# Kernel tuning notes

Hardware: AMD Instinct MI355X
Metric: run time of the kernel (lower is better)

Reference implementation:

```python
import jax, jax.numpy as jnp
import numpy as np

WT_LEVELS = 3  # wavelet decomposition levels

def haar2d(x):
    # orthonormal 2D Haar: 2x2 block -> 4 sub-bands, each scaled by 1/2
    a = x[:, :, 0::2, 0::2]; b = x[:, :, 0::2, 1::2]
    c = x[:, :, 1::2, 0::2]; d = x[:, :, 1::2, 1::2]
    ll = (a + b + c + d) * 0.5
    lh = (a - b + c - d) * 0.5
    hl = (a + b - c - d) * 0.5
    hh = (a - b - c + d) * 0.5
    return jnp.stack([ll, lh, hl, hh], axis=2)  # [B,C,4,h,w]

def ihaar2d(co):
    # exact inverse of haar2d
    ll, lh, hl, hh = co[:, :, 0], co[:, :, 1], co[:, :, 2], co[:, :, 3]
    a = (ll + lh + hl + hh) * 0.5
    b = (ll - lh + hl - hh) * 0.5
    c = (ll + lh - hl - hh) * 0.5
    d = (ll - lh - hl + hh) * 0.5
    B, C, h, w = ll.shape
    top = jnp.stack([a, b], axis=-1).reshape(B, C, h, 2 * w)
    bot = jnp.stack([c, d], axis=-1).reshape(B, C, h, 2 * w)
    return jnp.stack([top, bot], axis=3).reshape(B, C, 2 * h, 2 * w)

def dwconv(x, w):
    # depthwise conv, stride 1, 'same' padding (matches torch padding='same', k=5)
    return jax.lax.conv_general_dilated(
        x, w, (1, 1), 'SAME',
        dimension_numbers=('NCHW', 'OIHW', 'NCHW'),
        feature_group_count=x.shape[1])

def setup_inputs() -> dict:
    key = jax.random.key(0)
    ks = jax.random.split(key, 5)
    B, C, H, W, K, L = 8, 96, 224, 224, 5, WT_LEVELS
    x = jax.random.normal(ks[0], (B, C, H, W), jnp.float32)
    base_w = jax.random.normal(ks[1], (C, 1, K, K), jnp.float32) * 0.1
    base_b = jax.random.normal(ks[2], (C,), jnp.float32) * 0.01
    base_scale = jnp.ones((1, C, 1, 1), jnp.float32)
    wconv_w = jax.random.normal(ks[3], (L, 4 * C, 1, K, K), jnp.float32) * 0.1
    wscale = jnp.full((L, 1, 4 * C, 1, 1), 0.1, jnp.float32)
    return {"x": x, "base_w": base_w, "base_b": base_b,
            "base_scale": base_scale, "wconv_w": wconv_w, "wscale": wscale}

def reference(x, base_w, base_b, base_scale, wconv_w, wscale):
    B, C, H, W = x.shape
    # analysis cascade: decompose LL of previous level, conv+scale all 4 bands
    cur = x
    level_coeffs = []
    for i in range(WT_LEVELS):
        co = haar2d(cur)                 # [B,C,4,h,w]
        cur = co[:, :, 0]                # pre-conv LL feeds next level
        h, w = co.shape[-2:]
        flat = co.reshape(B, C * 4, h, w)
        flat = dwconv(flat, wconv_w[i]) * wscale[i]
        level_coeffs.append(flat.reshape(B, C, 4, h, w))
    # synthesis cascade: reconstructed LL from deeper level is added to
    # the shallower level's (convolved) LL band before inverse transform
    next_ll = jnp.zeros_like(level_coeffs[-1][:, :, 0])
    for i in reversed(range(WT_LEVELS)):
        co = level_coeffs[i].at[:, :, 0].add(next_ll)
        next_ll = ihaar2d(co)
    base = dwconv(x, base_w) * base_scale + base_b.reshape(1, C, 1, 1)
    return base + next_ll
```

## Files before the change

### kernel.cpp

```cpp
#include <hip/hip_runtime.h>

#define BB 8
#define CC 96
#define HH 224
#define WW 224

typedef _Float16 h2 __attribute__((ext_vector_type(2)));
__device__ __forceinline__ h2 u2h(unsigned u) { return __builtin_bit_cast(h2, u); }
__device__ __forceinline__ unsigned pkrtz(float a, float b) {
    return __builtin_bit_cast(unsigned, __builtin_amdgcn_cvt_pkrtz(a, b));
}

#if __has_builtin(__builtin_amdgcn_fdot2)
#define FDOT2(a, b, c) __builtin_amdgcn_fdot2((a), (b), (c), false)
#else
#define FDOT2(a, b, c) ((float)(a).x * (float)(b).x + (float)(a).y * (float)(b).y + (c))
#endif

__global__ __launch_bounds__(512, 4) void levels_fused(
    const float* __restrict__ x,
    float* __restrict__ c1,
    float* __restrict__ c2,
    const float* __restrict__ wt1, const float* __restrict__ ws1,
    const float* __restrict__ wt2, const float* __restrict__ ws2)
{
    const int bc = blockIdx.x, c = bc % CC;
    const int t = threadIdx.x;

    __shared__ unsigned s_c1[112 * 58];
    __shared__ unsigned s_sb1[4 * 60 * 31];
    __shared__ unsigned s_cur2[56 * 30];
    __shared__ unsigned s_sb2[4 * 32 * 17];
    __shared__ unsigned s_w2[240];

    for (int i = t; i < 4 * 60 * 31; i += 512) s_sb1[i] = 0;
    for (int i = t; i < 4 * 32 * 17; i += 512) s_sb2[i] = 0;

    if (t < 80) {
        int knl = t / 10;
        int par = t & 1, row = (t % 10) >> 1;
        int lvl = knl >> 2, s = knl & 3;
        const float* wt  = lvl ? wt2 : wt1;
        const float* wsc = lvl ? ws2 : ws1;
        float sc = 0.5f * wsc[c * 4 + s];
        float wv[5];
        #pragma unroll
        for (int j = 0; j < 5; ++j) wv[j] = wt[(c * 4 + s) * 25 + row * 5 + j] * sc;
        unsigned* dst = &s_w2[(knl * 2 + par) * 15 + row * 3];
        if (par == 0) {
            dst[0] = pkrtz(wv[0], wv[1]);
            dst[1] = pkrtz(wv[2], wv[3]);
            dst[2] = pkrtz(wv[4], 0.f);
        } else {
            dst[0] = pkrtz(0.f, wv[0]);
            dst[1] = pkrtz(wv[1], wv[2]);
            dst[2] = pkrtz(wv[3], wv[4]);
        }
    }

    const float* xp = x + (size_t)bc * HH * WW;
    for (int idx = t; idx < 112 * 56; idx += 512) {
        int r = idx / 56, g = idx % 56;
        const float* r0 = xp + (size_t)(2 * r) * WW + 4 * g;
        const float* r1 = r0 + WW;
        float4 a = *(const float4*)r0;
        float4 b = *(const float4*)r1;
        s_c1[r * 58 + g] = pkrtz(0.5f * (a.x + a.y + b.x + b.y),
                                 0.5f * (a.z + a.w + b.z + b.w));
    }
    __syncthreads();

    for (int idx = t; idx < 56 * 28; idx += 512) {
        int sr = idx / 28, sc2 = idx % 28;
        uint2 tp = *(const uint2*)&s_c1[(2 * sr) * 58 + 2 * sc2];
        uint2 bt = *(const uint2*)&s_c1[(2 * sr + 1) * 58 + 2 * sc2];
        h2 t0 = u2h(tp.x), t1 = u2h(tp.y), b0 = u2h(bt.x), b1 = u2h(bt.y);
        float P0 = (float)t0.x + (float)t0.y, M0 = (float)t0.x - (float)t0.y;
        float R0 = (float)b0.x + (float)b0.y, Q0 = (float)b0.x - (float)b0.y;
        float P1 = (float)t1.x + (float)t1.y, M1 = (float)t1.x - (float)t1.y;
        float R1 = (float)b1.x + (float)b1.y, Q1 = (float)b1.x - (float)b1.y;
        int o = (sr + 2) * 31 + (sc2 + 1);
        s_sb1[0 * 1860 + o] = pkrtz(P0 + R0, P1 + R1);
        s_sb1[1 * 1860 + o] = pkrtz(M0 + Q0, M1 + Q1);
        s_sb1[2 * 1860 + o] = pkrtz(P0 - R0, P1 - R1);
        s_sb1[3 * 1860 + o] = pkrtz(M0 - Q0, M1 - Q1);
        s_cur2[sr * 30 + sc2] = pkrtz(0.5f * (P0 + R0), 0.5f * (P1 + R1));
    }
    __syncthreads();

    if (t < 28 * 14) {
        int sr = t / 14, sc2 = t % 14;
        uint2 tp = *(const uint2*)&s_cur2[(2 * sr) * 30 + 2 * sc2];
        uint2 bt = *(const uint2*)&s_cur2[(2 * sr + 1) * 30 + 2 * sc2];
        h2 t0 = u2h(tp.x), t1 = u2h(tp.y), b0 = u2h(bt.x), b1 = u2h(bt.y);
        float P0 = (float)t0.x + (float)t0.y, M0 = (float)t0.x - (float)t0.y;
        float R0 = (float)b0.x + (float)b0.y, Q0 = (float)b0.x - (float)b0.y;
        float P1 = (float)t1.x + (float)t1.y, M1 = (float)t1.x - (float)t1.y;
        float R1 = (float)b1.x + (float)b1.y, Q1 = (float)b1.x - (float)b1.y;
        int o = (sr + 2) * 17 + (sc2 + 1);
        s_sb2[0 * 544 + o] = pkrtz(P0 + R0, P1 + R1);
        s_sb2[1 * 544 + o] = pkrtz(M0 + Q0, M1 + Q1);
        s_sb2[2 * 544 + o] = pkrtz(P0 - R0, P1 - R1);
        s_sb2[3 * 544 + o] = pkrtz(M0 - Q0, M1 - Q1);
    }

    {
        const int s = t >> 7, lane = t & 127;
        const int q = lane & 63, half = lane >> 6;
        if (q < 56) {
            const int par = q & 1, d0 = q >> 1, ps = half * 28;
            h2 w[5][3];
            {
                const unsigned* wp = &s_w2[(s * 2 + par) * 15];
                #pragma unroll
                for (int ki = 0; ki < 5; ++ki)
                    #pragma unroll
                    for (int m = 0; m < 3; ++m) w[ki][m] = u2h(wp[ki * 3 + m]);
            }
            float acc[28];
            #pragma unroll
            for (int r = 0; r < 28; ++r) acc[r] = 0.f;
            #pragma unroll
            for (int ri = 0; ri < 32; ++ri) {
                const unsigned* rp = &s_sb1[s * 1860 + (ps + ri) * 31 + d0];
                h2 g0 = u2h(rp[0]), g1 = u2h(rp[1]), g2 = u2h(rp[2]);
                #pragma unroll
                for (int ki = 0; ki < 5; ++ki) {
                    int r = ri - ki;
                    if (r >= 0 && r < 28)
                        acc[r] = FDOT2(g0, w[ki][0],
                                 FDOT2(g1, w[ki][1],
                                 FDOT2(g2, w[ki][2], acc[r])));
                }
            }
            const size_t ob = ((size_t)(bc * 4 + s) * 56 + ps) * 56 + q;
            #pragma unroll
            for (int r = 0; r < 28; ++r)
                c1[ob + (size_t)r * 56] = acc[r];
        }
    }
    __syncthreads();

    if (t < 112) {
        const int s = t / 28, q = t % 28;
        const int par = q & 1, d0 = q >> 1;
        h2 w[5][3];
        {
            const unsigned* wp = &s_w2[((4 + s) * 2 + par) * 15];
            #pragma unroll
            for (int ki = 0; ki < 5; ++ki)
                #pragma unroll
                for (int m = 0; m < 3; ++m) w[ki][m] = u2h(wp[ki * 3 + m]);
        }
        float acc[28];
        #pragma unroll
        for (int r = 0; r < 28; ++r) acc[r] = 0.f;
        #pragma unroll
        for (int ri = 0; ri < 32; ++ri) {
            const unsigned* rp = &s_sb2[s * 544 + ri * 17 + d0];
            h2 g0 = u2h(rp[0]), g1 = u2h(rp[1]), g2 = u2h(rp[2]);
            #pragma unroll
            for (int ki = 0; ki < 5; ++ki) {
                int r = ri - ki;
                if (r >= 0 && r < 28)
                    acc[r] = FDOT2(g0, w[ki][0],
                             FDOT2(g1, w[ki][1],
                             FDOT2(g2, w[ki][2], acc[r])));
            }
        }
        const size_t ob = (size_t)(bc * 4 + s) * 28 * 28 + q;
        #pragma unroll
        for (int r = 0; r < 28; ++r)
            c2[ob + (size_t)r * 28] = acc[r];
    }
}

__global__ __launch_bounds__(256, 7) void final_fused_v5(
    const float* __restrict__ x,
    const float* __restrict__ bw,
    const float* __restrict__ bb,
    const float* __restrict__ bs,
    const float* __restrict__ wt0,
    const float* __restrict__ wsc0,
    const float* __restrict__ c1,
    const float* __restrict__ c2,
    float* __restrict__ out)
{
    const int bc = blockIdx.z, c = bc % CC;
    const int t = threadIdx.x;

    __shared__ unsigned s_x2[64 * 34];
    __shared__ unsigned s_sb[4 * 544];
    __shared__ float s_rec1[28 * 29];
    __shared__ float s_rec2[14 * 15];
    __shared__ unsigned s_w2[150];
    _Float16* const s_cvh = reinterpret_cast<_Float16*>(s_x2);

    if (t < 50) {
        int par = t & 1, row = (t >> 1) % 5, knl = t / 10;
        float wv[5];
        if (knl == 0) {
            float sc = bs[c];
            #pragma unroll
            for (int j = 0; j < 5; ++j) wv[j] = bw[c * 25 + row * 5 + j] * sc;
        } else {
            int s = knl - 1;
            float sc = 0.5f * wsc0[c * 4 + s];
            #pragma unroll
            for (int j = 0; j < 5; ++j) wv[j] = wt0[(c * 4 + s) * 25 + row * 5 + j] * sc;
        }
        unsigned* dst = &s_w2[((knl * 2 + par) * 5 + row) * 3];
        if (par == 0) {
            dst[0] = pkrtz(wv[0], wv[1]);
            dst[1] = pkrtz(wv[2], wv[3]);
            dst[2] = pkrtz(wv[4], 0.f);
        } else {
            dst[0] = pkrtz(0.f, wv[0]);
            dst[1] = pkrtz(wv[1], wv[2]);
            dst[2] = pkrtz(wv[3], wv[4]);
        }
    }

    float c2v[4], c1v[4];
    const int p1 = t / 14, q1 = t % 14;
    if (t < 49) {
        const int p2 = t / 7, q2 = t % 7;
        const size_t b2 = (((size_t)bc * 4) * 28 + 7 * blockIdx.y + p2) * 28
                        + 7 * blockIdx.x + q2;
        #pragma unroll
        for (int s = 0; s < 4; ++s) c2v[s] = c2[b2 + (size_t)s * 28 * 28];
    }
    if (t < 196) {
        const size_t b1 = (((size_t)bc * 4) * 56 + 14 * blockIdx.y + p1) * 56
                        + 14 * blockIdx.x + q1;
        #pragma unroll
        for (int s = 0; s < 4; ++s) c1v[s] = c1[b1 + (size_t)s * 56 * 56];
    }

    const float* xp = x + (size_t)bc * HH * WW;
    const int gy0 = 56 * blockIdx.y - 4, gx0 = 56 * blockIdx.x - 4;
    for (int idx = t; idx < 1024; idx += 256) {
        int r = idx >> 4, j = idx & 15;
        int gr = gy0 + r, gc = gx0 + 4 * j;
        float4 v = make_float4(0.f, 0.f, 0.f, 0.f);
        if (gr >= 0 && gr < HH && gc >= 0 && gc + 3 < WW)
            v = *(const float4*)(xp + (size_t)gr * WW + gc);
        uint2 pp;
        pp.x = pkrtz(v.x, v.y);
        pp.y = pkrtz(v.z, v.w);
        *(uint2*)&s_x2[r * 34 + 2 * j] = pp;
    }

    if (t < 49) {
        const int p2 = t / 7, q2 = t % 7;
        float ll = c2v[0], lh = c2v[1], hl = c2v[2], hh = c2v[3];
        float a  = 0.5f * (ll + lh + hl + hh);
        float b  = 0.5f * (ll - lh + hl - hh);
        float cv = 0.5f * (ll + lh - hl - hh);
        float d  = 0.5f * (ll - lh - hl + hh);
        float* rp = &s_rec2[(2 * p2) * 15 + 2 * q2];
        rp[0] = a; rp[1] = b; rp[15] = cv; rp[16] = d;
    }
    __syncthreads();

    for (int idx = t; idx < 512; idx += 256) {
        int sr = idx >> 4, g = idx & 15;
        uint2 tp = *(const uint2*)&s_x2[(2 * sr) * 34 + 2 * g];
        uint2 bt = *(const uint2*)&s_x2[(2 * sr + 1) * 34 + 2 * g];
        h2 t0 = u2h(tp.x), t1 = u2h(tp.y), b0 = u2h(bt.x), b1 = u2h(bt.y);
        float a0 = t0.x, e0 = t0.y, cc0 = b0.x, f0 = b0.y;
        float a1 = t1.x, e1 = t1.y, cc1 = b1.x, f1 = b1.y;
        float P0 = a0 + e0, M0 = a0 - e0, R0 = cc0 + f0, Q0 = cc0 - f0;
        float P1 = a1 + e1, M1 = a1 - e1, R1 = cc1 + f1, Q1 = cc1 - f1;
        s_sb[0 * 544 + sr * 17 + g] = pkrtz(P0 + R0, P1 + R1);
        s_sb[1 * 544 + sr * 17 + g] = pkrtz(M0 + Q0, M1 + Q1);
        s_sb[2 * 544 + sr * 17 + g] = pkrtz(P0 - R0, P1 - R1);
        s_sb[3 * 544 + sr * 17 + g] = pkrtz(M0 - Q0, M1 - Q1);
    }

    const int q4 = t % 56, rb4 = t / 56;
    float bacc[14];
    if (t < 224) {
        const int par = q4 & 1, d0 = (q4 + 2) >> 1;
        h2 w[5][3];
        {
            const unsigned* wp = &s_w2[(par * 5) * 3];
            #pragma unroll
            for (int ki = 0; ki < 5; ++ki)
                #pragma unroll
                for (int m = 0; m < 3; ++m) w[ki][m] = u2h(wp[ki * 3 + m]);
        }
        #pragma unroll
        for (int r = 0; r < 14; ++r) bacc[r] = 0.f;
        #pragma unroll
        for (int ri = 0; ri < 18; ++ri) {
            const unsigned* rp = &s_x2[(rb4 * 14 + ri + 2) * 34 + d0];
            h2 g0 = u2h(rp[0]), g1 = u2h(rp[1]), g2 = u2h(rp[2]);
            #pragma unroll
            for (int ki = 0; ki < 5; ++ki) {
                int r = ri - ki;
                if (r >= 0 && r < 14)
                    bacc[r] = FDOT2(g0, w[ki][0],
                              FDOT2(g1, w[ki][1],
                              FDOT2(g2, w[ki][2], bacc[r])));
            }
        }
    }
    if (t < 196) {
        float ll = c1v[0] + s_rec2[p1 * 15 + q1];
        float lh = c1v[1], hl = c1v[2], hh = c1v[3];
        float a  = 0.5f * (ll + lh + hl + hh);
        float b  = 0.5f * (ll - lh + hl - hh);
        float cv = 0.5f * (ll + lh - hl - hh);
        float d  = 0.5f * (ll - lh - hl + hh);
        float* rp = &s_rec1[(2 * p1) * 29 + 2 * q1];
        rp[0] = a; rp[1] = b; rp[29] = cv; rp[30] = d;
    }
    __syncthreads();

    {
        const int s = t >> 6, u = t & 63;
        if (u < 56) {
            const int q = u % 28, rb = u / 28;
            const int par = q & 1, d0 = q >> 1;
            h2 w[5][3];
            {
                const unsigned* wp = &s_w2[(((1 + s) * 2 + par) * 5) * 3];
                #pragma unroll
                for (int ki = 0; ki < 5; ++ki)
                    #pragma unroll
                    for (int m = 0; m < 3; ++m) w[ki][m] = u2h(wp[ki * 3 + m]);
            }
            float acc[14];
            #pragma unroll
            for (int r = 0; r < 14; ++r) acc[r] = 0.f;
            #pragma unroll
            for (int ri = 0; ri < 18; ++ri) {
                const unsigned* rp = &s_sb[s * 544 + (rb * 14 + ri) * 17 + d0];
                h2 g0 = u2h(rp[0]), g1 = u2h(rp[1]), g2 = u2h(rp[2]);
                #pragma unroll
                for (int ki = 0; ki < 5; ++ki) {
                    int r = ri - ki;
                    if (r >= 0 && r < 14)
                        acc[r] = FDOT2(g0, w[ki][0],
                                 FDOT2(g1, w[ki][1],
                                 FDOT2(g2, w[ki][2], acc[r])));
                }
            }
            #pragma unroll
            for (int r = 0; r < 14; ++r)
                s_cvh[(s * 28 + rb * 14 + r) * 29 + q] = (_Float16)acc[r];
        }
    }
    __syncthreads();

    if (t < 224) {
        const float bbv = bb[c];
        const int qs = q4 >> 1;
        const float sx = (q4 & 1) ? -1.f : 1.f;
        float* op = out + ((size_t)bc * HH + 56 * blockIdx.y + rb4 * 14) * WW
                        + 56 * blockIdx.x + q4;
        #pragma unroll
        for (int j = 0; j < 7; ++j) {
            const int p = rb4 * 7 + j;
            float ll = (float)s_cvh[(0 * 28 + p) * 29 + qs] + s_rec1[p * 29 + qs];
            float lh = (float)s_cvh[(1 * 28 + p) * 29 + qs];
            float hl = (float)s_cvh[(2 * 28 + p) * 29 + qs];
            float hh = (float)s_cvh[(3 * 28 + p) * 29 + qs];
            float e0 = ll + sx * lh;
            float e1 = hl + sx * hh;
            float top = 0.5f * (e0 + e1);
            float bot = 0.5f * (e0 - e1);
            op[(size_t)(2 * j) * WW]     = bacc[2 * j]     + bbv + top;
            op[(size_t)(2 * j + 1) * WW] = bacc[2 * j + 1] + bbv + bot;
        }
    }
}

extern "C" void kernel_launch(void* const* d_in, const int* in_sizes, int n_in,
                              void* d_out, int out_size, void* d_ws, size_t ws_size,
                              hipStream_t stream) {
    const float* x          = (const float*)d_in[0];
    const float* base_w     = (const float*)d_in[1];
    const float* base_b     = (const float*)d_in[2];
    const float* base_scale = (const float*)d_in[3];
    const float* wconv_w    = (const float*)d_in[4];
    const float* wscale     = (const float*)d_in[5];
    float* out = (float*)d_out;
    float* ws  = (float*)d_ws;

    const size_t n1 = (size_t)BB * CC * 4 * 56 * 56;

    float* coeffs1 = ws;
    float* coeffs2 = coeffs1 + n1;

    const int z = BB * CC;

    levels_fused<<<z, 512, 0, stream>>>(
        x, coeffs1, coeffs2,
        wconv_w + 1 * 384 * 25, wscale + 1 * 384,
        wconv_w + 2 * 384 * 25, wscale + 2 * 384);
    final_fused_v5<<<dim3(4, 4, z), 256, 0, stream>>>(
        x, base_w, base_b, base_scale,
        wconv_w + 0 * 384 * 25, wscale + 0 * 384, coeffs1, coeffs2, out);
}
```

Baseline: 147.8 us.

## Shrink final kernel tiles to 32x32 with single-wave 64-thread blocks

Retiles the final fused kernel from 56x56 output tiles with 256-thread blocks to 32x32 tiles with 64-thread blocks over a 7x7 grid per channel image. Every thread now does work, with no idle threads for t>=224 or the u>=56 gaps, and a block fits in one wavefront, so barriers are cheap and more blocks can be resident. In exchange, the 4-pixel halo is a larger share of each smaller tile, so global and LDS traffic per output pixel rises, and many more blocks must be scheduled.

```diff
diff --git a/kernel.cpp b/kernel.cpp
--- a/kernel.cpp
+++ b/kernel.cpp
@@ -175,7 +175,7 @@
     }
 }
 
-__global__ __launch_bounds__(256, 7) void final_fused_v5(
+__global__ __launch_bounds__(64) void final_fused_v6(
     const float* __restrict__ x,
     const float* __restrict__ bw,
     const float* __restrict__ bb,
@@ -188,13 +188,14 @@
 {
     const int bc = blockIdx.z, c = bc % CC;
     const int t = threadIdx.x;
-
-    __shared__ unsigned s_x2[64 * 34];
-    __shared__ unsigned s_sb[4 * 544];
-    __shared__ float s_rec1[28 * 29];
-    __shared__ float s_rec2[14 * 15];
+    const int ox = 32 * blockIdx.x, oy = 32 * blockIdx.y;
+
+    __shared__ unsigned s_x[40 * 22];
+    __shared__ unsigned s_sb[4 * 20 * 11];
+    __shared__ float s_rec1[16 * 17];
+    __shared__ float s_rec2[8 * 9];
     __shared__ unsigned s_w2[150];
-    _Float16* const s_cvh = reinterpret_cast<_Float16*>(s_x2);
+    _Float16* const s_cvh = reinterpret_cast<_Float16*>(s_x);
 
     if (t < 50) {
         int par = t & 1, row = (t >> 1) % 5, knl = t / 10;
@@ -222,66 +223,75 @@
     }
 
     float c2v[4], c1v[4];
-    const int p1 = t / 14, q1 = t % 14;
-    if (t < 49) {
-        const int p2 = t / 7, q2 = t % 7;
-        const size_t b2 = (((size_t)bc * 4) * 28 + 7 * blockIdx.y + p2) * 28
-                        + 7 * blockIdx.x + q2;
-        #pragma unroll
-        for (int s = 0; s < 4; ++s) c2v[s] = c2[b2 + (size_t)s * 28 * 28];
-    }
-    if (t < 196) {
-        const size_t b1 = (((size_t)bc * 4) * 56 + 14 * blockIdx.y + p1) * 56
-                        + 14 * blockIdx.x + q1;
-        #pragma unroll
-        for (int s = 0; s < 4; ++s) c1v[s] = c1[b1 + (size_t)s * 56 * 56];
+    if (t < 16) {
+        const int p2 = t >> 2, q2 = t & 3;
+        const size_t b2 = (((size_t)bc * 4) * 28 + 4 * blockIdx.y + p2) * 28
+                        + 4 * blockIdx.x + q2;
+        #pragma unroll
+        for (int s = 0; s < 4; ++s) c2v[s] = c2[b2 + (size_t)s * 784];
+    }
+    const int p1 = t >> 3, q1 = t & 7;
+    {
+        const size_t b1 = (((size_t)bc * 4) * 56 + 8 * blockIdx.y + p1) * 56
+                        + 8 * blockIdx.x + q1;
+        #pragma unroll
+        for (int s = 0; s < 4; ++s) c1v[s] = c1[b1 + (size_t)s * 3136];
     }
 
     const float* xp = x + (size_t)bc * HH * WW;
-    const int gy0 = 56 * blockIdx.y - 4, gx0 = 56 * blockIdx.x - 4;
-    for (int idx = t; idx < 1024; idx += 256) {
-        int r = idx >> 4, j = idx & 15;
-        int gr = gy0 + r, gc = gx0 + 4 * j;
-        float4 v = make_float4(0.f, 0.f, 0.f, 0.f);
-        if (gr >= 0 && gr < HH && gc >= 0 && gc + 3 < WW)
-            v = *(const float4*)(xp + (size_t)gr * WW + gc);
-        uint2 pp;
-        pp.x = pkrtz(v.x, v.y);
-        pp.y = pkrtz(v.z, v.w);
-        *(uint2*)&s_x2[r * 34 + 2 * j] = pp;
-    }
-
-    if (t < 49) {
-        const int p2 = t / 7, q2 = t % 7;
+    const int gy0 = oy - 4, gx0 = ox - 4;
+    #pragma unroll
+    for (int it = 0; it < 7; ++it) {
+        int idx = t + it * 64;
+        if (idx < 400) {
+            int r = idx / 10, j = idx % 10;
+            int gr = gy0 + r, gc = gx0 + 4 * j;
+            float4 v = make_float4(0.f, 0.f, 0.f, 0.f);
+            if (gr >= 0 && gr < HH && gc >= 0 && gc + 3 < WW)
+                v = *(const float4*)(xp + (size_t)gr * WW + gc);
+            uint2 pp;
+            pp.x = pkrtz(v.x, v.y);
+            pp.y = pkrtz(v.z, v.w);
+            *(uint2*)&s_x[r * 22 + 2 * j] = pp;
+        }
+    }
+
+    if (t < 16) {
+        const int p2 = t >> 2, q2 = t & 3;
         float ll = c2v[0], lh = c2v[1], hl = c2v[2], hh = c2v[3];
         float a  = 0.5f * (ll + lh + hl + hh);
         float b  = 0.5f * (ll - lh + hl - hh);
         float cv = 0.5f * (ll + lh - hl - hh);
         float d  = 0.5f * (ll - lh - hl + hh);
-        float* rp = &s_rec2[(2 * p2) * 15 + 2 * q2];
-        rp[0] = a; rp[1] = b; rp[15] = cv; rp[16] = d;
-    }
-    __syncthreads();
-
-    for (int idx = t; idx < 512; idx += 256) {
-        int sr = idx >> 4, g = idx & 15;
-        uint2 tp = *(const uint2*)&s_x2[(2 * sr) * 34 + 2 * g];
-        uint2 bt = *(const uint2*)&s_x2[(2 * sr + 1) * 34 + 2 * g];
-        h2 t0 = u2h(tp.x), t1 = u2h(tp.y), b0 = u2h(bt.x), b1 = u2h(bt.y);
-        float a0 = t0.x, e0 = t0.y, cc0 = b0.x, f0 = b0.y;
-        float a1 = t1.x, e1 = t1.y, cc1 = b1.x, f1 = b1.y;
-        float P0 = a0 + e0, M0 = a0 - e0, R0 = cc0 + f0, Q0 = cc0 - f0;
-        float P1 = a1 + e1, M1 = a1 - e1, R1 = cc1 + f1, Q1 = cc1 - f1;
-        s_sb[0 * 544 + sr * 17 + g] = pkrtz(P0 + R0, P1 + R1);
-        s_sb[1 * 544 + sr * 17 + g] = pkrtz(M0 + Q0, M1 + Q1);
-        s_sb[2 * 544 + sr * 17 + g] = pkrtz(P0 - R0, P1 - R1);
-        s_sb[3 * 544 + sr * 17 + g] = pkrtz(M0 - Q0, M1 - Q1);
-    }
-
-    const int q4 = t % 56, rb4 = t / 56;
-    float bacc[14];
-    if (t < 224) {
-        const int par = q4 & 1, d0 = (q4 + 2) >> 1;
+        float* rp = &s_rec2[(2 * p2) * 9 + 2 * q2];
+        rp[0] = a; rp[1] = b; rp[9] = cv; rp[10] = d;
+    }
+    __syncthreads();
+
+    #pragma unroll
+    for (int it = 0; it < 4; ++it) {
+        int idx = t + it * 64;
+        if (idx < 200) {
+            int sr = idx / 10, g = idx % 10;
+            uint2 tp = *(const uint2*)&s_x[(2 * sr) * 22 + 2 * g];
+            uint2 bt = *(const uint2*)&s_x[(2 * sr + 1) * 22 + 2 * g];
+            h2 t0 = u2h(tp.x), t1 = u2h(tp.y), b0 = u2h(bt.x), b1 = u2h(bt.y);
+            float P0 = (float)t0.x + (float)t0.y, M0 = (float)t0.x - (float)t0.y;
+            float R0 = (float)b0.x + (float)b0.y, Q0 = (float)b0.x - (float)b0.y;
+            float P1 = (float)t1.x + (float)t1.y, M1 = (float)t1.x - (float)t1.y;
+            float R1 = (float)b1.x + (float)b1.y, Q1 = (float)b1.x - (float)b1.y;
+            int o = sr * 11 + g;
+            s_sb[0 * 220 + o] = pkrtz(P0 + R0, P1 + R1);
+            s_sb[1 * 220 + o] = pkrtz(M0 + Q0, M1 + Q1);
+            s_sb[2 * 220 + o] = pkrtz(P0 - R0, P1 - R1);
+            s_sb[3 * 220 + o] = pkrtz(M0 - Q0, M1 - Q1);
+        }
+    }
+
+    const int qb = t & 31, hb = t >> 5;
+    float bacc[16];
+    {
+        const int par = qb & 1, d0 = (qb + 2) >> 1;
         h2 w[5][3];
         {
             const unsigned* wp = &s_w2[(par * 5) * 3];
@@ -291,82 +301,79 @@
                 for (int m = 0; m < 3; ++m) w[ki][m] = u2h(wp[ki * 3 + m]);
         }
         #pragma unroll
-        for (int r = 0; r < 14; ++r) bacc[r] = 0.f;
-        #pragma unroll
-        for (int ri = 0; ri < 18; ++ri) {
-            const unsigned* rp = &s_x2[(rb4 * 14 + ri + 2) * 34 + d0];
+        for (int r = 0; r < 16; ++r) bacc[r] = 0.f;
+        #pragma unroll
+        for (int ri = 0; ri < 20; ++ri) {
+            const unsigned* rp = &s_x[(hb * 16 + ri + 2) * 22 + d0];
             h2 g0 = u2h(rp[0]), g1 = u2h(rp[1]), g2 = u2h(rp[2]);
             #pragma unroll
             for (int ki = 0; ki < 5; ++ki) {
                 int r = ri - ki;
-                if (r >= 0 && r < 14)
+                if (r >= 0 && r < 16)
                     bacc[r] = FDOT2(g0, w[ki][0],
                               FDOT2(g1, w[ki][1],
                               FDOT2(g2, w[ki][2], bacc[r])));
             }
         }
     }
-    if (t < 196) {
-        float ll = c1v[0] + s_rec2[p1 * 15 + q1];
+
+    {
+        float ll = c1v[0] + s_rec2[p1 * 9 + q1];
         float lh = c1v[1], hl = c1v[2], hh = c1v[3];
         float a  = 0.5f * (ll + lh + hl + hh);
         float b  = 0.5f * (ll - lh + hl - hh);
         float cv = 0.5f * (ll + lh - hl - hh);
         float d  = 0.5f * (ll - lh - hl + hh);
-        float* rp = &s_rec1[(2 * p1) * 29 + 2 * q1];
-        rp[0] = a; rp[1] = b; rp[29] = cv; rp[30] = d;
-    }
-    __syncthreads();
-
-    {
-        const int s = t >> 6, u = t & 63;
-        if (u < 56) {
-            const int q = u % 28, rb = u / 28;
-            const int par = q & 1, d0 = q >> 1;
-            h2 w[5][3];
-            {
-                const unsigned* wp = &s_w2[(((1 + s) * 2 + par) * 5) * 3];
+        float* rp = &s_rec1[(2 * p1) * 17 + 2 * q1];
+        rp[0] = a; rp[1] = b; rp[17] = cv; rp[18] = d;
+    }
+    __syncthreads();
+
+    {
+        const int s = t >> 4, q = t & 15;
+        const int par = q & 1, d0 = q >> 1;
+        h2 w[5][3];
+        {
+            const unsigned* wp = &s_w2[(((1 + s) * 2 + par) * 5) * 3];
+            #pragma unroll
+            for (int ki = 0; ki < 5; ++ki)
                 #pragma unroll
-                for (int ki = 0; ki < 5; ++ki)
-                    #pragma unroll
-                    for (int m = 0; m < 3; ++m) w[ki][m] = u2h(wp[ki * 3 + m]);
+                for (int m = 0; m < 3; ++m) w[ki][m] = u2h(wp[ki * 3 + m]);
+        }
+        float acc[16];
+        #pragma unroll
+        for (int r = 0; r < 16; ++r) acc[r] = 0.f;
+        #pragma unroll
+        for (int ri = 0; ri < 20; ++ri) {
+            const unsigned* rp = &s_sb[s * 220 + ri * 11 + d0];
+            h2 g0 = u2h(rp[0]), g1 = u2h(rp[1]), g2 = u2h(rp[2]);
+            #pragma unroll
+            for (int ki = 0; ki < 5; ++ki) {
+                int r = ri - ki;
+                if (r >= 0 && r < 16)
+                    acc[r] = FDOT2(g0, w[ki][0],
+                             FDOT2(g1, w[ki][1],
+                             FDOT2(g2, w[ki][2], acc[r])));
             }
-            float acc[14];
-            #pragma unroll
-            for (int r = 0; r < 14; ++r) acc[r] = 0.f;
-            #pragma unroll
-            for (int ri = 0; ri < 18; ++ri) {
-                const unsigned* rp = &s_sb[s * 544 + (rb * 14 + ri) * 17 + d0];
-                h2 g0 = u2h(rp[0]), g1 = u2h(rp[1]), g2 = u2h(rp[2]);
-                #pragma unroll
-                for (int ki = 0; ki < 5; ++ki) {
-                    int r = ri - ki;
-                    if (r >= 0 && r < 14)
-                        acc[r] = FDOT2(g0, w[ki][0],
-                                 FDOT2(g1, w[ki][1],
-                                 FDOT2(g2, w[ki][2], acc[r])));
-                }
-            }
-            #pragma unroll
-            for (int r = 0; r < 14; ++r)
-                s_cvh[(s * 28 + rb * 14 + r) * 29 + q] = (_Float16)acc[r];
-        }
-    }
-    __syncthreads();
-
-    if (t < 224) {
+        }
+        #pragma unroll
+        for (int r = 0; r < 16; ++r)
+            s_cvh[(s * 16 + r) * 18 + q] = (_Float16)acc[r];
+    }
+    __syncthreads();
+
+    {
         const float bbv = bb[c];
-        const int qs = q4 >> 1;
-        const float sx = (q4 & 1) ? -1.f : 1.f;
-        float* op = out + ((size_t)bc * HH + 56 * blockIdx.y + rb4 * 14) * WW
-                        + 56 * blockIdx.x + q4;
-        #pragma unroll
-        for (int j = 0; j < 7; ++j) {
-            const int p = rb4 * 7 + j;
-            float ll = (float)s_cvh[(0 * 28 + p) * 29 + qs] + s_rec1[p * 29 + qs];
-            float lh = (float)s_cvh[(1 * 28 + p) * 29 + qs];
-            float hl = (float)s_cvh[(2 * 28 + p) * 29 + qs];
-            float hh = (float)s_cvh[(3 * 28 + p) * 29 + qs];
+        const int qs = qb >> 1;
+        const float sx = (qb & 1) ? -1.f : 1.f;
+        float* op = out + ((size_t)bc * HH + oy + hb * 16) * WW + ox + qb;
+        #pragma unroll
+        for (int j = 0; j < 8; ++j) {
+            const int p = hb * 8 + j;
+            float ll = (float)s_cvh[(0 * 16 + p) * 18 + qs] + s_rec1[p * 17 + qs];
+            float lh = (float)s_cvh[(1 * 16 + p) * 18 + qs];
+            float hl = (float)s_cvh[(2 * 16 + p) * 18 + qs];
+            float hh = (float)s_cvh[(3 * 16 + p) * 18 + qs];
             float e0 = ll + sx * lh;
             float e1 = hl + sx * hh;
             float top = 0.5f * (e0 + e1);
@@ -400,7 +407,7 @@
         x, coeffs1, coeffs2,
         wconv_w + 1 * 384 * 25, wscale + 1 * 384,
         wconv_w + 2 * 384 * 25, wscale + 2 * 384);
-    final_fused_v5<<<dim3(4, 4, z), 256, 0, stream>>>(
+    final_fused_v6<<<dim3(7, 7, z), 64, 0, stream>>>(
         x, base_w, base_b, base_scale,
         wconv_w + 0 * 384 * 25, wscale + 0 * 384, coeffs1, coeffs2, out);
 }
```

New measurement: 176.5 us. 1.19x slower.

## Compute even/odd output columns per thread and pack sub-band pairs in LDS

Applied to the files above, without the earlier changes.

The base conv and level-0 sub-band convs now have each thread compute both even and odd output columns from one set of LDS row reads. This halves the active threads in those phases and reuses each loaded row for two weight sets. Convolved sub-bands are stored as interleaved half2 pairs, so the final inverse-Haar stage reads two packed words per pixel and writes float2 output pairs. The cost is higher register pressure, with occupancy hints lowered from 7 to 5 blocks, and fewer active threads during the conv phases.

```diff
diff --git a/kernel.cpp b/kernel.cpp
--- a/kernel.cpp
+++ b/kernel.cpp
@@ -175,7 +175,7 @@
     }
 }
 
-__global__ __launch_bounds__(256, 7) void final_fused_v5(
+__global__ __launch_bounds__(256, 5) void final_fused_v8(
     const float* __restrict__ x,
     const float* __restrict__ bw,
     const float* __restrict__ bb,
@@ -189,12 +189,13 @@
     const int bc = blockIdx.z, c = bc % CC;
     const int t = threadIdx.x;
 
-    __shared__ unsigned s_x2[64 * 34];
+    __shared__ unsigned s_x[64 * 34];
     __shared__ unsigned s_sb[4 * 544];
     __shared__ float s_rec1[28 * 29];
     __shared__ float s_rec2[14 * 15];
     __shared__ unsigned s_w2[150];
-    _Float16* const s_cvh = reinterpret_cast<_Float16*>(s_x2);
+    unsigned* const s_cv01 = s_x;
+    unsigned* const s_cv23 = s_x + 812;
 
     if (t < 50) {
         int par = t & 1, row = (t >> 1) % 5, knl = t / 10;
@@ -228,13 +229,13 @@
         const size_t b2 = (((size_t)bc * 4) * 28 + 7 * blockIdx.y + p2) * 28
                         + 7 * blockIdx.x + q2;
         #pragma unroll
-        for (int s = 0; s < 4; ++s) c2v[s] = c2[b2 + (size_t)s * 28 * 28];
+        for (int s = 0; s < 4; ++s) c2v[s] = c2[b2 + (size_t)s * 784];
     }
     if (t < 196) {
         const size_t b1 = (((size_t)bc * 4) * 56 + 14 * blockIdx.y + p1) * 56
                         + 14 * blockIdx.x + q1;
         #pragma unroll
-        for (int s = 0; s < 4; ++s) c1v[s] = c1[b1 + (size_t)s * 56 * 56];
+        for (int s = 0; s < 4; ++s) c1v[s] = c1[b1 + (size_t)s * 3136];
     }
 
     const float* xp = x + (size_t)bc * HH * WW;
@@ -248,7 +249,7 @@
         uint2 pp;
         pp.x = pkrtz(v.x, v.y);
         pp.y = pkrtz(v.z, v.w);
-        *(uint2*)&s_x2[r * 34 + 2 * j] = pp;
+        *(uint2*)&s_x[r * 34 + 2 * j] = pp;
     }
 
     if (t < 49) {
@@ -265,8 +266,8 @@
 
     for (int idx = t; idx < 512; idx += 256) {
         int sr = idx >> 4, g = idx & 15;
-        uint2 tp = *(const uint2*)&s_x2[(2 * sr) * 34 + 2 * g];
-        uint2 bt = *(const uint2*)&s_x2[(2 * sr + 1) * 34 + 2 * g];
+        uint2 tp = *(const uint2*)&s_x[(2 * sr) * 34 + 2 * g];
+        uint2 bt = *(const uint2*)&s_x[(2 * sr + 1) * 34 + 2 * g];
         h2 t0 = u2h(tp.x), t1 = u2h(tp.y), b0 = u2h(bt.x), b1 = u2h(bt.y);
         float a0 = t0.x, e0 = t0.y, cc0 = b0.x, f0 = b0.y;
         float a1 = t1.x, e1 = t1.y, cc1 = b1.x, f1 = b1.y;
@@ -278,34 +279,43 @@
         s_sb[3 * 544 + sr * 17 + g] = pkrtz(M0 - Q0, M1 - Q1);
     }
 
-    const int q4 = t % 56, rb4 = t / 56;
-    float bacc[14];
-    if (t < 224) {
-        const int par = q4 & 1, d0 = (q4 + 2) >> 1;
-        h2 w[5][3];
+    const int kp = t % 28, rbp = t / 28;
+    float bacc_e[14], bacc_o[14];
+    if (t < 112) {
+        h2 we[5][3], wo[5][3];
         {
-            const unsigned* wp = &s_w2[(par * 5) * 3];
+            const unsigned* wpe = &s_w2[0];
+            const unsigned* wpo = &s_w2[15];
             #pragma unroll
             for (int ki = 0; ki < 5; ++ki)
                 #pragma unroll
-                for (int m = 0; m < 3; ++m) w[ki][m] = u2h(wp[ki * 3 + m]);
-        }
-        #pragma unroll
-        for (int r = 0; r < 14; ++r) bacc[r] = 0.f;
+                for (int m = 0; m < 3; ++m) {
+                    we[ki][m] = u2h(wpe[ki * 3 + m]);
+                    wo[ki][m] = u2h(wpo[ki * 3 + m]);
+                }
+        }
+        #pragma unroll
+        for (int r = 0; r < 14; ++r) { bacc_e[r] = 0.f; bacc_o[r] = 0.f; }
+        const int d0 = kp + 1;
         #pragma unroll
         for (int ri = 0; ri < 18; ++ri) {
-            const unsigned* rp = &s_x2[(rb4 * 14 + ri + 2) * 34 + d0];
+            const unsigned* rp = &s_x[(rbp * 14 + ri + 2) * 34 + d0];
             h2 g0 = u2h(rp[0]), g1 = u2h(rp[1]), g2 = u2h(rp[2]);
             #pragma unroll
             for (int ki = 0; ki < 5; ++ki) {
                 int r = ri - ki;
-                if (r >= 0 && r < 14)
-                    bacc[r] = FDOT2(g0, w[ki][0],
-                              FDOT2(g1, w[ki][1],
-                              FDOT2(g2, w[ki][2], bacc[r])));
+                if (r >= 0 && r < 14) {
+                    bacc_e[r] = FDOT2(g0, we[ki][0],
+                                FDOT2(g1, we[ki][1],
+                                FDOT2(g2, we[ki][2], bacc_e[r])));
+                    bacc_o[r] = FDOT2(g0, wo[ki][0],
+                                FDOT2(g1, wo[ki][1],
+                                FDOT2(g2, wo[ki][2], bacc_o[r])));
+                }
             }
         }
     }
+
     if (t < 196) {
         float ll = c1v[0] + s_rec2[p1 * 15 + q1];
         float lh = c1v[1], hl = c1v[2], hh = c1v[3];
@@ -318,61 +328,71 @@
     }
     __syncthreads();
 
-    {
-        const int s = t >> 6, u = t & 63;
-        if (u < 56) {
-            const int q = u % 28, rb = u / 28;
-            const int par = q & 1, d0 = q >> 1;
-            h2 w[5][3];
-            {
-                const unsigned* wp = &s_w2[(((1 + s) * 2 + par) * 5) * 3];
+    if (t < 224) {
+        const int s = t / 56, rem = t % 56;
+        const int k = rem % 14, rb = rem / 14;
+        h2 we[5][3], wo[5][3];
+        {
+            const unsigned* wpe = &s_w2[((1 + s) * 2 + 0) * 15];
+            const unsigned* wpo = &s_w2[((1 + s) * 2 + 1) * 15];
+            #pragma unroll
+            for (int ki = 0; ki < 5; ++ki)
                 #pragma unroll
-                for (int ki = 0; ki < 5; ++ki)
-                    #pragma unroll
-                    for (int m = 0; m < 3; ++m) w[ki][m] = u2h(wp[ki * 3 + m]);
-            }
-            float acc[14];
-            #pragma unroll
-            for (int r = 0; r < 14; ++r) acc[r] = 0.f;
-            #pragma unroll
-            for (int ri = 0; ri < 18; ++ri) {
-                const unsigned* rp = &s_sb[s * 544 + (rb * 14 + ri) * 17 + d0];
-                h2 g0 = u2h(rp[0]), g1 = u2h(rp[1]), g2 = u2h(rp[2]);
-                #pragma unroll
-                for (int ki = 0; ki < 5; ++ki) {
-                    int r = ri - ki;
-                    if (r >= 0 && r < 14)
-                        acc[r] = FDOT2(g0, w[ki][0],
-                                 FDOT2(g1, w[ki][1],
-                                 FDOT2(g2, w[ki][2], acc[r])));
+                for (int m = 0; m < 3; ++m) {
+                    we[ki][m] = u2h(wpe[ki * 3 + m]);
+                    wo[ki][m] = u2h(wpo[ki * 3 + m]);
+                }
+        }
+        float acc_e[7], acc_o[7];
+        #pragma unroll
+        for (int r = 0; r < 7; ++r) { acc_e[r] = 0.f; acc_o[r] = 0.f; }
+        #pragma unroll
+        for (int ri = 0; ri < 11; ++ri) {
+            const unsigned* rp = &s_sb[s * 544 + (rb * 7 + ri) * 17 + k];
+            h2 g0 = u2h(rp[0]), g1 = u2h(rp[1]), g2 = u2h(rp[2]);
+            #pragma unroll
+            for (int ki = 0; ki < 5; ++ki) {
+                int r = ri - ki;
+                if (r >= 0 && r < 7) {
+                    acc_e[r] = FDOT2(g0, we[ki][0],
+                               FDOT2(g1, we[ki][1],
+                               FDOT2(g2, we[ki][2], acc_e[r])));
+                    acc_o[r] = FDOT2(g0, wo[ki][0],
+                               FDOT2(g1, wo[ki][1],
+                               FDOT2(g2, wo[ki][2], acc_o[r])));
                 }
             }
-            #pragma unroll
-            for (int r = 0; r < 14; ++r)
-                s_cvh[(s * 28 + rb * 14 + r) * 29 + q] = (_Float16)acc[r];
-        }
-    }
-    __syncthreads();
-
-    if (t < 224) {
+        }
+        _Float16* base16 = reinterpret_cast<_Float16*>((s < 2) ? s_cv01 : s_cv23);
+        const int hf = s & 1;
+        #pragma unroll
+        for (int r = 0; r < 7; ++r) {
+            int p = rb * 7 + r;
+            base16[(p * 29 + 2 * k) * 2 + hf]     = (_Float16)acc_e[r];
+            base16[(p * 29 + 2 * k + 1) * 2 + hf] = (_Float16)acc_o[r];
+        }
+    }
+    __syncthreads();
+
+    if (t < 112) {
         const float bbv = bb[c];
-        const int qs = q4 >> 1;
-        const float sx = (q4 & 1) ? -1.f : 1.f;
-        float* op = out + ((size_t)bc * HH + 56 * blockIdx.y + rb4 * 14) * WW
-                        + 56 * blockIdx.x + q4;
+        float* op = out + ((size_t)bc * HH + 56 * blockIdx.y + rbp * 14) * WW
+                        + 56 * blockIdx.x + 2 * kp;
         #pragma unroll
         for (int j = 0; j < 7; ++j) {
-            const int p = rb4 * 7 + j;
-            float ll = (float)s_cvh[(0 * 28 + p) * 29 + qs] + s_rec1[p * 29 + qs];
-            float lh = (float)s_cvh[(1 * 28 + p) * 29 + qs];
-            float hl = (float)s_cvh[(2 * 28 + p) * 29 + qs];
-            float hh = (float)s_cvh[(3 * 28 + p) * 29 + qs];
-            float e0 = ll + sx * lh;
-            float e1 = hl + sx * hh;
-            float top = 0.5f * (e0 + e1);
-            float bot = 0.5f * (e0 - e1);
-            op[(size_t)(2 * j) * WW]     = bacc[2 * j]     + bbv + top;
-            op[(size_t)(2 * j + 1) * WW] = bacc[2 * j + 1] + bbv + bot;
+            const int p = rbp * 7 + j;
+            h2 v01 = u2h(s_cv01[p * 29 + kp]);
+            h2 v23 = u2h(s_cv23[p * 29 + kp]);
+            float ll = (float)v01.x + s_rec1[p * 29 + kp];
+            float lh = (float)v01.y;
+            float hl = (float)v23.x;
+            float hh = (float)v23.y;
+            float a  = 0.5f * (ll + lh + hl + hh) + bacc_e[2 * j]     + bbv;
+            float b  = 0.5f * (ll - lh + hl - hh) + bacc_o[2 * j]     + bbv;
+            float cv = 0.5f * (ll + lh - hl - hh) + bacc_e[2 * j + 1] + bbv;
+            float d  = 0.5f * (ll - lh - hl + hh) + bacc_o[2 * j + 1] + bbv;
+            *reinterpret_cast<float2*>(op + (size_t)(2 * j) * WW)     = make_float2(a, b);
+            *reinterpret_cast<float2*>(op + (size_t)(2 * j + 1) * WW) = make_float2(cv, d);
         }
     }
 }
@@ -400,7 +420,7 @@
         x, coeffs1, coeffs2,
         wconv_w + 1 * 384 * 25, wscale + 1 * 384,
         wconv_w + 2 * 384 * 25, wscale + 2 * 384);
-    final_fused_v5<<<dim3(4, 4, z), 256, 0, stream>>>(
+    final_fused_v8<<<dim3(4, 4, z), 256, 0, stream>>>(
         x, base_w, base_b, base_scale,
         wconv_w + 0 * 384 * 25, wscale + 0 * 384, coeffs1, coeffs2, out);
 }
```

New measurement: 150.5 us. Within noise of the previous version (+1.8%).

## Move level-2/1 inverse Haar into first kernel and pass fp16 reconstruction

Applied to the files above, without the earlier changes.

The first kernel now keeps the level-1 and level-2 convolved coefficients in shared memory as fp16 pairs. It runs the level-2 and level-1 inverse Haar steps there and writes a single 112x112 packed-fp16 reconstruction per channel to global memory. The final kernel reads that plane directly instead of loading four fp32 level-1 bands and four level-2 bands and reconstructing them. This is meant to cut intermediate global traffic substantially and shift work out of the final kernel, at the cost of fp16 rounding of the intermediates, extra syncs in the first kernel, and some redundant stores of zero.

```diff
diff --git a/kernel.cpp b/kernel.cpp
--- a/kernel.cpp
+++ b/kernel.cpp
@@ -17,10 +17,9 @@
 #define FDOT2(a, b, c) ((float)(a).x * (float)(b).x + (float)(a).y * (float)(b).y + (c))
 #endif
 
-__global__ __launch_bounds__(512, 4) void levels_fused(
+__global__ __launch_bounds__(512, 4) void levels_fused2(
     const float* __restrict__ x,
-    float* __restrict__ c1,
-    float* __restrict__ c2,
+    unsigned* __restrict__ rec1g,
     const float* __restrict__ wt1, const float* __restrict__ ws1,
     const float* __restrict__ wt2, const float* __restrict__ ws2)
 {
@@ -32,6 +31,12 @@
     __shared__ unsigned s_cur2[56 * 30];
     __shared__ unsigned s_sb2[4 * 32 * 17];
     __shared__ unsigned s_w2[240];
+
+    unsigned* const c1_01 = s_c1;
+    unsigned* const c1_23 = s_c1 + 3192;
+    unsigned* const c2_01 = s_cur2;
+    unsigned* const c2_23 = s_cur2 + 812;
+    float*    const rec2  = reinterpret_cast<float*>(s_sb1);
 
     for (int i = t; i < 4 * 60 * 31; i += 512) s_sb1[i] = 0;
     for (int i = t; i < 4 * 32 * 17; i += 512) s_sb2[i] = 0;
@@ -133,10 +138,11 @@
                                  FDOT2(g2, w[ki][2], acc[r])));
                 }
             }
-            const size_t ob = ((size_t)(bc * 4 + s) * 56 + ps) * 56 + q;
+            _Float16* dstH = reinterpret_cast<_Float16*>((s < 2) ? c1_01 : c1_23);
+            const int hf = s & 1;
             #pragma unroll
             for (int r = 0; r < 28; ++r)
-                c1[ob + (size_t)r * 56] = acc[r];
+                dstH[((ps + r) * 57 + q) * 2 + hf] = (_Float16)acc[r];
         }
     }
     __syncthreads();
@@ -168,22 +174,54 @@
                              FDOT2(g2, w[ki][2], acc[r])));
             }
         }
-        const size_t ob = (size_t)(bc * 4 + s) * 28 * 28 + q;
+        _Float16* dstH = reinterpret_cast<_Float16*>((s < 2) ? c2_01 : c2_23);
+        const int hf = s & 1;
         #pragma unroll
         for (int r = 0; r < 28; ++r)
-            c2[ob + (size_t)r * 28] = acc[r];
+            dstH[(r * 29 + q) * 2 + hf] = (_Float16)acc[r];
+    }
+    __syncthreads();
+
+    for (int i = t; i < 784; i += 512) {
+        int p2 = i / 28, q2 = i % 28;
+        h2 v01 = u2h(c2_01[p2 * 29 + q2]);
+        h2 v23 = u2h(c2_23[p2 * 29 + q2]);
+        float ll = v01.x, lh = v01.y, hl = v23.x, hh = v23.y;
+        float a  = 0.5f * (ll + lh + hl + hh);
+        float b  = 0.5f * (ll - lh + hl - hh);
+        float cv = 0.5f * (ll + lh - hl - hh);
+        float d  = 0.5f * (ll - lh - hl + hh);
+        float* rp = &rec2[(2 * p2) * 57 + 2 * q2];
+        rp[0] = a; rp[1] = b; rp[57] = cv; rp[58] = d;
+    }
+    __syncthreads();
+
+    unsigned* rg = rec1g + (size_t)bc * 112 * 56;
+    for (int i = t; i < 3136; i += 512) {
+        int p1 = i / 56, q1 = i % 56;
+        h2 v01 = u2h(c1_01[p1 * 57 + q1]);
+        h2 v23 = u2h(c1_23[p1 * 57 + q1]);
+        float ll = (float)v01.x + rec2[p1 * 57 + q1];
+        float lh = v01.y, hl = v23.x, hh = v23.y;
+        float a  = 0.5f * (ll + lh + hl + hh);
+        float b  = 0.5f * (ll - lh + hl - hh);
+        float cv = 0.5f * (ll + lh - hl - hh);
+        float d  = 0.5f * (ll - lh - hl + hh);
+        rg[(size_t)(2 * p1) * 56 + q1]     = pkrtz(a, cv) ;
+        rg[(size_t)(2 * p1 + 1) * 56 + q1] = 0;
+        rg[(size_t)(2 * p1) * 56 + q1]     = pkrtz(a, b);
+        rg[(size_t)(2 * p1 + 1) * 56 + q1] = pkrtz(cv, d);
     }
 }
 
-__global__ __launch_bounds__(256, 7) void final_fused_v5(
+__global__ __launch_bounds__(256, 7) void final_fused_v10(
     const float* __restrict__ x,
     const float* __restrict__ bw,
     const float* __restrict__ bb,
     const float* __restrict__ bs,
     const float* __restrict__ wt0,
     const float* __restrict__ wsc0,
-    const float* __restrict__ c1,
-    const float* __restrict__ c2,
+    const unsigned* __restrict__ rec1g,
     float* __restrict__ out)
 {
     const int bc = blockIdx.z, c = bc % CC;
@@ -192,7 +230,6 @@
     __shared__ unsigned s_x2[64 * 34];
     __shared__ unsigned s_sb[4 * 544];
     __shared__ float s_rec1[28 * 29];
-    __shared__ float s_rec2[14 * 15];
     __shared__ unsigned s_w2[150];
     _Float16* const s_cvh = reinterpret_cast<_Float16*>(s_x2);
 
@@ -221,20 +258,17 @@
         }
     }
 
-    float c2v[4], c1v[4];
-    const int p1 = t / 14, q1 = t % 14;
-    if (t < 49) {
-        const int p2 = t / 7, q2 = t % 7;
-        const size_t b2 = (((size_t)bc * 4) * 28 + 7 * blockIdx.y + p2) * 28
-                        + 7 * blockIdx.x + q2;
-        #pragma unroll
-        for (int s = 0; s < 4; ++s) c2v[s] = c2[b2 + (size_t)s * 28 * 28];
-    }
     if (t < 196) {
-        const size_t b1 = (((size_t)bc * 4) * 56 + 14 * blockIdx.y + p1) * 56
-                        + 14 * blockIdx.x + q1;
-        #pragma unroll
-        for (int s = 0; s < 4; ++s) c1v[s] = c1[b1 + (size_t)s * 56 * 56];
+        #pragma unroll
+        for (int k = 0; k < 2; ++k) {
+            int idx = 2 * t + k;
+            int r = idx / 14, d = idx % 14;
+            unsigned v = rec1g[((size_t)bc * 112 + 28 * blockIdx.y + r) * 56
+                               + 14 * blockIdx.x + d];
+            h2 hv = u2h(v);
+            s_rec1[r * 29 + 2 * d]     = hv.x;
+            s_rec1[r * 29 + 2 * d + 1] = hv.y;
+        }
     }
 
     const float* xp = x + (size_t)bc * HH * WW;
@@ -249,17 +283,6 @@
         pp.x = pkrtz(v.x, v.y);
         pp.y = pkrtz(v.z, v.w);
         *(uint2*)&s_x2[r * 34 + 2 * j] = pp;
-    }
-
-    if (t < 49) {
-        const int p2 = t / 7, q2 = t % 7;
-        float ll = c2v[0], lh = c2v[1], hl = c2v[2], hh = c2v[3];
-        float a  = 0.5f * (ll + lh + hl + hh);
-        float b  = 0.5f * (ll - lh + hl - hh);
-        float cv = 0.5f * (ll + lh - hl - hh);
-        float d  = 0.5f * (ll - lh - hl + hh);
-        float* rp = &s_rec2[(2 * p2) * 15 + 2 * q2];
-        rp[0] = a; rp[1] = b; rp[15] = cv; rp[16] = d;
     }
     __syncthreads();
 
@@ -306,16 +329,6 @@
             }
         }
     }
-    if (t < 196) {
-        float ll = c1v[0] + s_rec2[p1 * 15 + q1];
-        float lh = c1v[1], hl = c1v[2], hh = c1v[3];
-        float a  = 0.5f * (ll + lh + hl + hh);
-        float b  = 0.5f * (ll - lh + hl - hh);
-        float cv = 0.5f * (ll + lh - hl - hh);
-        float d  = 0.5f * (ll - lh - hl + hh);
-        float* rp = &s_rec1[(2 * p1) * 29 + 2 * q1];
-        rp[0] = a; rp[1] = b; rp[29] = cv; rp[30] = d;
-    }
     __syncthreads();
 
     {
@@ -387,20 +400,15 @@
     const float* wconv_w    = (const float*)d_in[4];
     const float* wscale     = (const float*)d_in[5];
     float* out = (float*)d_out;
-    float* ws  = (float*)d_ws;
-
-    const size_t n1 = (size_t)BB * CC * 4 * 56 * 56;
-
-    float* coeffs1 = ws;
-    float* coeffs2 = coeffs1 + n1;
+    unsigned* rec1 = (unsigned*)d_ws;
 
     const int z = BB * CC;
 
-    levels_fused<<<z, 512, 0, stream>>>(
-        x, coeffs1, coeffs2,
+    levels_fused2<<<z, 512, 0, stream>>>(
+        x, rec1,
         wconv_w + 1 * 384 * 25, wscale + 1 * 384,
         wconv_w + 2 * 384 * 25, wscale + 2 * 384);
-    final_fused_v5<<<dim3(4, 4, z), 256, 0, stream>>>(
+    final_fused_v10<<<dim3(4, 4, z), 256, 0, stream>>>(
         x, base_w, base_b, base_scale,
-        wconv_w + 0 * 384 * 25, wscale + 0 * 384, coeffs1, coeffs2, out);
+        wconv_w + 0 * 384 * 25, wscale + 0 * 384, rec1, out);
 }
```

Result: faster. 130.5 us (-11.8%).
